# Performance work log

Hardware: AMD Instinct MI355X
Metric: run time of the kernel (lower is better)

## Reference

```python
import jax, jax.numpy as jnp
import numpy as np

B, S, C = 4, 2048, 1024
E, H = 1024, 16
D = E // H  # head_dim = 64


def setup_inputs() -> dict:
    key = jax.random.key(0)
    k1, k2, k3, k4, k5 = jax.random.split(key, 5)
    s = 1.0 / np.sqrt(C)
    return {
        "x": jax.random.normal(k1, (B, S, C), dtype=jnp.float32),
        "w_qkv": jax.random.uniform(k2, (C, 3 * E), minval=-s, maxval=s, dtype=jnp.float32),
        "b_qkv": jax.random.uniform(k3, (3 * E,), minval=-s, maxval=s, dtype=jnp.float32),
        "w_out": jax.random.uniform(k4, (E, E), minval=-1.0 / np.sqrt(E), maxval=1.0 / np.sqrt(E), dtype=jnp.float32),
        "b_out": jax.random.uniform(k5, (E,), minval=-1.0 / np.sqrt(E), maxval=1.0 / np.sqrt(E), dtype=jnp.float32),
    }


def reference(x, w_qkv, b_qkv, w_out, b_out):
    b, s, _ = x.shape
    qkv = x @ w_qkv + b_qkv                      # [B,S,3E]
    qkv = qkv.reshape(b, s, 3, H, D)
    q = qkv[:, :, 0].transpose(0, 2, 1, 3)       # [B,H,S,D]
    k = qkv[:, :, 1].transpose(0, 2, 1, 3)
    v = qkv[:, :, 2].transpose(0, 2, 1, 3)
    scale = jnp.asarray(D, x.dtype) ** 0.5
    scores = jnp.einsum("bhqd,bhkd->bhqk", q, k) / scale
    attn = jax.nn.softmax(scores, axis=-1)       # dropout is identity in eval mode
    out = jnp.einsum("bhqk,bhkd->bhqd", attn, v)
    out = out.transpose(0, 2, 1, 3).reshape(b, s, E)
    return out @ w_out + b_out
```

## Files before the change

### kernel.cpp

```cpp
#include <hip/hip_runtime.h>


typedef _Float16 f16;
typedef f16 f16x2 __attribute__((ext_vector_type(2)));
typedef f16 f16x4 __attribute__((ext_vector_type(4)));
typedef f16 f16x8 __attribute__((ext_vector_type(8)));
typedef float f32x4 __attribute__((ext_vector_type(4)));

typedef const __attribute__((address_space(1))) void* gas_ptr;
typedef __attribute__((address_space(3))) void* lds_ptr;

__device__ __forceinline__ void load_lds16(const void* g, void* s) {
  __builtin_amdgcn_global_load_lds((gas_ptr)g, (lds_ptr)s, 16, 0, 0);
}

__device__ __forceinline__ f32x4 mfma16(f16x8 a, f16x8 b, f32x4 c) {
  return __builtin_amdgcn_mfma_f32_16x16x32_f16(a, b, c, 0, 0, 0);
}

__device__ __forceinline__ f16x2 pk2(float a, float b) {
  return __builtin_bit_cast(f16x2, __builtin_amdgcn_cvt_pkrtz(a, b));
}

__global__ __launch_bounds__(256) void prep(const float* __restrict__ x, f16* __restrict__ xh,
                                            const float* __restrict__ w_qkv, f16* __restrict__ wqkvT,
                                            const float* __restrict__ w_out, f16* __restrict__ woutT) {
  __shared__ float t[32][33];
  int bid = blockIdx.x, tid = threadIdx.x;
  if (bid < 4096) {
    long i = (long)bid * 256 + tid;
    const float4* p = (const float4*)x;
    float4 a = p[2 * i], b = p[2 * i + 1];
    f16x8 o;
    o[0] = (f16)a.x; o[1] = (f16)a.y; o[2] = (f16)a.z; o[3] = (f16)a.w;
    o[4] = (f16)b.x; o[5] = (f16)b.y; o[6] = (f16)b.z; o[7] = (f16)b.w;
    *(f16x8*)(xh + 8 * i) = o;
    return;
  }
  const float* in;
  f16* out;
  int R, C, c0, r0;
  if (bid < 7168) {
    int r = bid - 4096;
    in = w_qkv; out = wqkvT; R = 1024; C = 3072;
    c0 = (r % 96) * 32; r0 = (r / 96) * 32;
  } else {
    int r = bid - 7168;
    in = w_out; out = woutT; R = 1024; C = 1024;
    c0 = (r & 31) * 32; r0 = (r >> 5) * 32;
  }
  int tx = tid & 31, ty = tid >> 5;
#pragma unroll
  for (int j = 0; j < 4; ++j)
    t[ty + 8 * j][tx] = in[(long)(r0 + ty + 8 * j) * C + c0 + tx];
  __syncthreads();
#pragma unroll
  for (int j = 0; j < 4; ++j)
    out[(long)(c0 + ty + 8 * j) * R + r0 + tx] = (f16)t[tx][ty + 8 * j];
}

__global__ __launch_bounds__(256) void qkv_gemm(const f16* __restrict__ A, const f16* __restrict__ BT,
                                                const float* __restrict__ bias,
                                                f16* __restrict__ Qs, f16* __restrict__ Kk,
                                                f16* __restrict__ Vt) {
  __shared__ __align__(16) f16 lA[2][128 * 64];
  __shared__ __align__(16) f16 lB[2][128 * 64];
  const int K = 1024;
  int tid = threadIdx.x, w = tid >> 6, lane = tid & 63, l16 = lane & 15, quad = lane >> 4;
  int wm = (w >> 1) * 64, wn = (w & 1) * 64;
  int id = blockIdx.y * gridDim.x + blockIdx.x;
  int xcd = id & 7, cch = id >> 3;
  int bx = xcd * 8 + (cch & 7), by = cch >> 3;
  int blockM = bx * 128, blockN = by * 128;
  int sw = l16 & 7;
  f32x4 acc[4][4] = {};

  auto stage = [&](int kt) {
    int k0 = kt * 64;
    f16* dA = lA[kt & 1];
    f16* dB = lB[kt & 1];
#pragma unroll
    for (int i = 0; i < 4; ++i) {
      int c = i * 256 + tid;
      int row = c >> 3;
      int sc = (c & 7) ^ (row & 7);
      load_lds16(A + (long)(blockM + row) * K + k0 + sc * 8, dA + c * 8);
      load_lds16(BT + (long)(blockN + row) * K + k0 + sc * 8, dB + c * 8);
    }
  };

  stage(0);
  asm volatile("s_waitcnt vmcnt(0)" ::: "memory");
  __builtin_amdgcn_s_barrier();

  for (int t = 0; t < 16; ++t) {
    if (t < 15) stage(t + 1);
    const f16* cA = lA[t & 1];
    const f16* cB = lB[t & 1];
#pragma unroll
    for (int ks = 0; ks < 2; ++ks) {
      f16x8 af[4], bf[4];
#pragma unroll
      for (int mb = 0; mb < 4; ++mb)
        af[mb] = *(const f16x8*)&cA[(wm + mb * 16 + l16) * 64 + ((ks * 4 + quad) ^ sw) * 8];
#pragma unroll
      for (int nb = 0; nb < 4; ++nb)
        bf[nb] = *(const f16x8*)&cB[(wn + nb * 16 + l16) * 64 + ((ks * 4 + quad) ^ sw) * 8];
      __builtin_amdgcn_s_setprio(1);
#pragma unroll
      for (int mb = 0; mb < 4; ++mb)
#pragma unroll
        for (int nb = 0; nb < 4; ++nb)
          acc[mb][nb] = mfma16(af[mb], bf[nb], acc[mb][nb]);
      __builtin_amdgcn_s_setprio(0);
    }
    asm volatile("s_waitcnt vmcnt(0)" ::: "memory");
    __builtin_amdgcn_s_barrier();
  }

  int which = by >> 3;
  const float SCALE = 0.18033688011112042f;
#pragma unroll
  for (int nb = 0; nb < 4; ++nb) {
    int col = blockN + wn + nb * 16 + l16;
    int hd = col & 1023, h = hd >> 6, d = hd & 63;
    float bv = bias[col];
#pragma unroll
    for (int mb = 0; mb < 4; ++mb) {
      int row0 = blockM + wm + mb * 16 + quad * 4;
      int b = row0 >> 11, s0 = row0 & 2047;
      if (which == 2) {
        f16x2 a = pk2(acc[mb][nb][0] + bv, acc[mb][nb][1] + bv);
        f16x2 c = pk2(acc[mb][nb][2] + bv, acc[mb][nb][3] + bv);
        *(f16x4*)&Vt[((b * 16 + h) * 64 + d) * 2048 + s0] =
            __builtin_shufflevector(a, c, 0, 1, 2, 3);
      } else if (which == 0) {
#pragma unroll
        for (int r = 0; r < 4; ++r)
          Qs[((b * 16 + h) * 2048 + s0 + r) * 64 + d] = (f16)((acc[mb][nb][r] + bv) * SCALE);
      } else {
#pragma unroll
        for (int r = 0; r < 4; ++r)
          Kk[((b * 16 + h) * 2048 + s0 + r) * 64 + d] = (f16)(acc[mb][nb][r] + bv);
      }
    }
  }
}

__global__ __launch_bounds__(512, 4) void attn(const f16* __restrict__ Qs, const f16* __restrict__ Kk,
                                               const f16* __restrict__ Vt, f16* __restrict__ ctx) {
  __shared__ __align__(16) f16 lK[2][64 * 64];
  __shared__ __align__(16) f16 lV[2][64 * 64];
  int id = blockIdx.y * gridDim.x + blockIdx.x;
  int swz = (id & 7) * 64 + (id >> 3);
  int qt = swz & 7, bh = swz >> 3;
  int tid = threadIdx.x, lane = tid & 63, l16 = lane & 15, quad = lane >> 4;
  int w = tid >> 6;
  int swr = l16 & 7;
  const f16* Qbase = Qs + ((long)bh * 2048 + qt * 256 + w * 32) * 64;
  const f16* Kbh = Kk + (long)bh * 2048 * 64;
  const f16* Vbh = Vt + (long)bh * 64 * 2048;

  f16x8 qf[2][2];
#pragma unroll
  for (int rb = 0; rb < 2; ++rb)
#pragma unroll
    for (int ks = 0; ks < 2; ++ks)
      qf[rb][ks] = *(const f16x8*)(Qbase + (rb * 16 + l16) * 64 + ks * 32 + quad * 8);

  f32x4 of[2][4] = {};
  f32x4 osum[2] = {};
  const f16 one = (f16)1.f;
  const f16x8 vone8 = {one, one, one, one, one, one, one, one};

  int rs = tid >> 3, o = (tid & 7) * 8, c1 = tid & 7;
  int jj = rs & 7;
  int koff = o & 31;
  int Lp = (o & 32) + ((koff & 12) << 1) + ((koff >> 4) << 2);
  int pv0b = (((Lp >> 3) ^ jj) << 4) + ((Lp & 4) << 1);
  int pv1b = ((((Lp >> 3) + 1) ^ jj) << 4) + ((Lp & 4) << 1);

  auto stageK = [&](int kt) {
    int kb0 = kt * 64;
    f16* dst = lK[kt & 1];
    load_lds16(Kbh + (kb0 + rs) * 64 + (c1 ^ jj) * 8, dst + tid * 8);
  };
  auto writeV = [&](int buf, float4 va) {
    f16* d0 = lV[buf] + rs * 64;
    f16x8 a8 = __builtin_bit_cast(f16x8, va);
    *(f16x4*)((char*)d0 + pv0b) = __builtin_shufflevector(a8, a8, 0, 1, 2, 3);
    *(f16x4*)((char*)d0 + pv1b) = __builtin_shufflevector(a8, a8, 4, 5, 6, 7);
  };

  {
    stageK(0);
    float4 va = *(const float4*)(Vbh + (long)rs * 2048 + o);
    writeV(0, va);
    asm volatile("s_waitcnt vmcnt(0)" ::: "memory");
    __builtin_amdgcn_s_barrier();
  }

  for (int kt = 0; kt < 32; ++kt) {
    int cur = kt & 1, nxt = cur ^ 1;

    float4 va;
    if (kt < 31) {
      int kb0 = (kt + 1) * 64;
      stageK(kt + 1);
      va = *(const float4*)(Vbh + (long)rs * 2048 + kb0 + o);
    }

    __builtin_amdgcn_s_setprio(1);
#pragma unroll
    for (int kp = 0; kp < 2; ++kp) {
      f16x4 pah[2][2];
#pragma unroll
      for (int kbh = 0; kbh < 2; ++kbh) {
        int kb = kp * 2 + kbh;
        f16x8 kf0 = *(const f16x8*)&lK[cur][(kb * 16 + l16) * 64 + ((quad ^ swr) << 3)];
        f16x8 kf1 = *(const f16x8*)&lK[cur][(kb * 16 + l16) * 64 + (((4 + quad) ^ swr) << 3)];
#pragma unroll
        for (int rb = 0; rb < 2; ++rb) {
          f32x4 z = {};
          z = mfma16(kf0, qf[rb][0], z);
          z = mfma16(kf1, qf[rb][1], z);
          float p0 = __builtin_amdgcn_exp2f(z[0]);
          float p1 = __builtin_amdgcn_exp2f(z[1]);
          float p2 = __builtin_amdgcn_exp2f(z[2]);
          float p3 = __builtin_amdgcn_exp2f(z[3]);
          pah[rb][kbh] = __builtin_shufflevector(pk2(p0, p1), pk2(p2, p3), 0, 1, 2, 3);
        }
      }
      f16x8 pa[2];
      pa[0] = __builtin_shufflevector(pah[0][0], pah[0][1], 0, 1, 2, 3, 4, 5, 6, 7);
      pa[1] = __builtin_shufflevector(pah[1][0], pah[1][1], 0, 1, 2, 3, 4, 5, 6, 7);

#pragma unroll
      for (int db = 0; db < 4; ++db) {
        f16x8 vf = *(const f16x8*)&lV[cur][(db * 16 + l16) * 64 + (((kp * 4 + quad) ^ swr) << 3)];
#pragma unroll
        for (int rb = 0; rb < 2; ++rb)
          of[rb][db] = mfma16(pa[rb], vf, of[rb][db]);
      }
#pragma unroll
      for (int rb = 0; rb < 2; ++rb)
        osum[rb] = mfma16(pa[rb], vone8, osum[rb]);
    }
    __builtin_amdgcn_s_setprio(0);

    if (kt < 31) {
      writeV(nxt, va);
      asm volatile("s_waitcnt vmcnt(0)" ::: "memory");
      __builtin_amdgcn_s_barrier();
    }
  }

  int b = bh >> 4, h = bh & 15;
  long token0 = (long)b * 2048 + qt * 256 + w * 32;
#pragma unroll
  for (int rb = 0; rb < 2; ++rb) {
    float inv[4];
#pragma unroll
    for (int r = 0; r < 4; ++r) inv[r] = 1.0f / osum[rb][r];
#pragma unroll
    for (int db = 0; db < 4; ++db)
#pragma unroll
      for (int r = 0; r < 4; ++r)
        ctx[(token0 + rb * 16 + quad * 4 + r) * 1024 + h * 64 + db * 16 + l16] =
            (f16)(of[rb][db][r] * inv[r]);
  }
}

__global__ __launch_bounds__(256) void proj_gemm(const f16* __restrict__ A, const f16* __restrict__ BT,
                                                 const float* __restrict__ bias,
                                                 float* __restrict__ out) {
  __shared__ __align__(16) f16 lA[2][128 * 64];
  __shared__ __align__(16) f16 lB[2][128 * 64];
  const int K = 1024;
  int tid = threadIdx.x, w = tid >> 6, lane = tid & 63, l16 = lane & 15, quad = lane >> 4;
  int wm = (w >> 1) * 64, wn = (w & 1) * 64;
  int id = blockIdx.y * gridDim.x + blockIdx.x;
  int xcd = id & 7, cch = id >> 3;
  int bx = xcd * 8 + (cch & 7), by = cch >> 3;
  int blockM = bx * 128, blockN = by * 128;
  int sw = l16 & 7;
  f32x4 acc[4][4] = {};

  auto stage = [&](int kt) {
    int k0 = kt * 64;
    f16* dA = lA[kt & 1];
    f16* dB = lB[kt & 1];
#pragma unroll
    for (int i = 0; i < 4; ++i) {
      int c = i * 256 + tid;
      int row = c >> 3;
      int sc = (c & 7) ^ (row & 7);
      load_lds16(A + (long)(blockM + row) * K + k0 + sc * 8, dA + c * 8);
      load_lds16(BT + (long)(blockN + row) * K + k0 + sc * 8, dB + c * 8);
    }
  };

  stage(0);
  asm volatile("s_waitcnt vmcnt(0)" ::: "memory");
  __builtin_amdgcn_s_barrier();

  for (int t = 0; t < 16; ++t) {
    if (t < 15) stage(t + 1);
    const f16* cA = lA[t & 1];
    const f16* cB = lB[t & 1];
#pragma unroll
    for (int ks = 0; ks < 2; ++ks) {
      f16x8 af[4], bf[4];
#pragma unroll
      for (int mb = 0; mb < 4; ++mb)
        af[mb] = *(const f16x8*)&cA[(wm + mb * 16 + l16) * 64 + ((ks * 4 + quad) ^ sw) * 8];
#pragma unroll
      for (int nb = 0; nb < 4; ++nb)
        bf[nb] = *(const f16x8*)&cB[(wn + nb * 16 + l16) * 64 + ((ks * 4 + quad) ^ sw) * 8];
      __builtin_amdgcn_s_setprio(1);
#pragma unroll
      for (int mb = 0; mb < 4; ++mb)
#pragma unroll
        for (int nb = 0; nb < 4; ++nb)
          acc[mb][nb] = mfma16(af[mb], bf[nb], acc[mb][nb]);
      __builtin_amdgcn_s_setprio(0);
    }
    asm volatile("s_waitcnt vmcnt(0)" ::: "memory");
    __builtin_amdgcn_s_barrier();
  }

#pragma unroll
  for (int nb = 0; nb < 4; ++nb) {
    int col = blockN + wn + nb * 16 + l16;
    float bv = bias[col];
#pragma unroll
    for (int mb = 0; mb < 4; ++mb) {
#pragma unroll
      for (int r = 0; r < 4; ++r) {
        int row = blockM + wm + mb * 16 + quad * 4 + r;
        out[(long)row * 1024 + col] = acc[mb][nb][r] + bv;
      }
    }
  }
}

extern "C" void kernel_launch(void* const* d_in, const int* in_sizes, int n_in,
                              void* d_out, int out_size, void* d_ws, size_t ws_size,
                              hipStream_t stream) {
  const float* x     = (const float*)d_in[0];
  const float* w_qkv = (const float*)d_in[1];
  const float* b_qkv = (const float*)d_in[2];
  const float* w_out = (const float*)d_in[3];
  const float* b_out = (const float*)d_in[4];
  float* out = (float*)d_out;

  char* ws = (char*)d_ws;
  f16* xh    = (f16*)(ws);
  f16* ctx   = (f16*)(ws);
  f16* wqkvT = (f16*)(ws + 16777216);
  f16* woutT = (f16*)(ws + 23068672);
  f16* Qs    = (f16*)(ws + 25165824);
  f16* Kk    = (f16*)(ws + 41943040);
  f16* Vt    = (f16*)(ws + 58720256);

  prep<<<8192, 256, 0, stream>>>(x, xh, w_qkv, wqkvT, w_out, woutT);
  qkv_gemm<<<dim3(64, 24), 256, 0, stream>>>(xh, wqkvT, b_qkv, Qs, Kk, Vt);
  attn<<<dim3(8, 64), 512, 0, stream>>>(Qs, Kk, Vt, ctx);
  proj_gemm<<<dim3(64, 8), 256, 0, stream>>>(ctx, woutT, b_out, out);
}
```

Measured before the change: 254.0 us.

## Use 8-wave blocks for GEMMs and 128-key tiles with register-staged K in attention

Both GEMM kernels now launch 512 threads per 128x128 tile, each wave computing a 32x64 sub-tile, to raise wave count and latency hiding. The attention kernel doubles its K/V tile to 128 keys, halving the number of loop iterations and barriers. It also replaces the direct global-to-LDS K load with register loads followed by LDS writes. The cost is more LDS per block, which may limit occupancy, and a longer register-held prefetch of four float4 values per thread.

```diff
diff --git a/kernel.cpp b/kernel.cpp
--- a/kernel.cpp
+++ b/kernel.cpp
@@ -59,29 +59,29 @@
     out[(long)(c0 + ty + 8 * j) * R + r0 + tx] = (f16)t[tx][ty + 8 * j];
 }
 
-__global__ __launch_bounds__(256) void qkv_gemm(const f16* __restrict__ A, const f16* __restrict__ BT,
-                                                const float* __restrict__ bias,
-                                                f16* __restrict__ Qs, f16* __restrict__ Kk,
-                                                f16* __restrict__ Vt) {
+__global__ __launch_bounds__(512, 4) void qkv_gemm(const f16* __restrict__ A, const f16* __restrict__ BT,
+                                                   const float* __restrict__ bias,
+                                                   f16* __restrict__ Qs, f16* __restrict__ Kk,
+                                                   f16* __restrict__ Vt) {
   __shared__ __align__(16) f16 lA[2][128 * 64];
   __shared__ __align__(16) f16 lB[2][128 * 64];
   const int K = 1024;
   int tid = threadIdx.x, w = tid >> 6, lane = tid & 63, l16 = lane & 15, quad = lane >> 4;
-  int wm = (w >> 1) * 64, wn = (w & 1) * 64;
+  int wm = (w >> 1) * 32, wn = (w & 1) * 64;
   int id = blockIdx.y * gridDim.x + blockIdx.x;
   int xcd = id & 7, cch = id >> 3;
   int bx = xcd * 8 + (cch & 7), by = cch >> 3;
   int blockM = bx * 128, blockN = by * 128;
   int sw = l16 & 7;
-  f32x4 acc[4][4] = {};
+  f32x4 acc[2][4] = {};
 
   auto stage = [&](int kt) {
     int k0 = kt * 64;
     f16* dA = lA[kt & 1];
     f16* dB = lB[kt & 1];
 #pragma unroll
-    for (int i = 0; i < 4; ++i) {
-      int c = i * 256 + tid;
+    for (int i = 0; i < 2; ++i) {
+      int c = i * 512 + tid;
       int row = c >> 3;
       int sc = (c & 7) ^ (row & 7);
       load_lds16(A + (long)(blockM + row) * K + k0 + sc * 8, dA + c * 8);
@@ -99,16 +99,16 @@
     const f16* cB = lB[t & 1];
 #pragma unroll
     for (int ks = 0; ks < 2; ++ks) {
-      f16x8 af[4], bf[4];
-#pragma unroll
-      for (int mb = 0; mb < 4; ++mb)
+      f16x8 af[2], bf[4];
+#pragma unroll
+      for (int mb = 0; mb < 2; ++mb)
         af[mb] = *(const f16x8*)&cA[(wm + mb * 16 + l16) * 64 + ((ks * 4 + quad) ^ sw) * 8];
 #pragma unroll
       for (int nb = 0; nb < 4; ++nb)
         bf[nb] = *(const f16x8*)&cB[(wn + nb * 16 + l16) * 64 + ((ks * 4 + quad) ^ sw) * 8];
       __builtin_amdgcn_s_setprio(1);
 #pragma unroll
-      for (int mb = 0; mb < 4; ++mb)
+      for (int mb = 0; mb < 2; ++mb)
 #pragma unroll
         for (int nb = 0; nb < 4; ++nb)
           acc[mb][nb] = mfma16(af[mb], bf[nb], acc[mb][nb]);
@@ -126,7 +126,7 @@
     int hd = col & 1023, h = hd >> 6, d = hd & 63;
     float bv = bias[col];
 #pragma unroll
-    for (int mb = 0; mb < 4; ++mb) {
+    for (int mb = 0; mb < 2; ++mb) {
       int row0 = blockM + wm + mb * 16 + quad * 4;
       int b = row0 >> 11, s0 = row0 & 2047;
       if (which == 2) {
@@ -149,8 +149,8 @@
 
 __global__ __launch_bounds__(512, 4) void attn(const f16* __restrict__ Qs, const f16* __restrict__ Kk,
                                                const f16* __restrict__ Vt, f16* __restrict__ ctx) {
-  __shared__ __align__(16) f16 lK[2][64 * 64];
-  __shared__ __align__(16) f16 lV[2][64 * 64];
+  __shared__ __align__(16) f16 lK[2][128 * 64];
+  __shared__ __align__(16) f16 lV[2][64 * 128];
   int id = blockIdx.y * gridDim.x + blockIdx.x;
   int swz = (id & 7) * 64 + (id >> 3);
   int qt = swz & 7, bh = swz >> 3;
@@ -173,46 +173,52 @@
   const f16 one = (f16)1.f;
   const f16x8 vone8 = {one, one, one, one, one, one, one, one};
 
-  int rs = tid >> 3, o = (tid & 7) * 8, c1 = tid & 7;
-  int jj = rs & 7;
+  int rk0 = tid >> 3, cl = tid & 7;
+  int jjk = rk0 & 7;
+  int kCl = (cl ^ jjk) * 8;
+  int dv0 = tid >> 4, ck = tid & 15, o = ck * 8;
+  int jjv = dv0 & 7;
   int koff = o & 31;
-  int Lp = (o & 32) + ((koff & 12) << 1) + ((koff >> 4) << 2);
-  int pv0b = (((Lp >> 3) ^ jj) << 4) + ((Lp & 4) << 1);
-  int pv1b = ((((Lp >> 3) + 1) ^ jj) << 4) + ((Lp & 4) << 1);
-
-  auto stageK = [&](int kt) {
-    int kb0 = kt * 64;
-    f16* dst = lK[kt & 1];
-    load_lds16(Kbh + (kb0 + rs) * 64 + (c1 ^ jj) * 8, dst + tid * 8);
+  int Lp = (o & 96) + ((koff & 12) << 1) + ((koff >> 4) << 2);
+  int pv0b = (((Lp >> 3) ^ jjv) << 4) + ((Lp & 4) << 1);
+  int pv1b = ((((Lp >> 3) + 1) ^ jjv) << 4) + ((Lp & 4) << 1);
+
+  auto loadKV = [&](int kt, float4& ka, float4& kb_, float4& va, float4& vb) {
+    int kb0 = kt * 128;
+    ka  = *(const float4*)(Kbh + (kb0 + rk0) * 64 + cl * 8);
+    kb_ = *(const float4*)(Kbh + (kb0 + rk0 + 64) * 64 + cl * 8);
+    va  = *(const float4*)(Vbh + (long)dv0 * 2048 + kb0 + o);
+    vb  = *(const float4*)(Vbh + (long)(dv0 + 32) * 2048 + kb0 + o);
   };
-  auto writeV = [&](int buf, float4 va) {
-    f16* d0 = lV[buf] + rs * 64;
+  auto writeKV = [&](int buf, float4 ka, float4 kb_, float4 va, float4 vb) {
+    *(f16x8*)&lK[buf][rk0 * 64 + kCl] = __builtin_bit_cast(f16x8, ka);
+    *(f16x8*)&lK[buf][(rk0 + 64) * 64 + kCl] = __builtin_bit_cast(f16x8, kb_);
+    char* d0 = (char*)(lV[buf] + dv0 * 128);
+    char* d1 = (char*)(lV[buf] + (dv0 + 32) * 128);
     f16x8 a8 = __builtin_bit_cast(f16x8, va);
-    *(f16x4*)((char*)d0 + pv0b) = __builtin_shufflevector(a8, a8, 0, 1, 2, 3);
-    *(f16x4*)((char*)d0 + pv1b) = __builtin_shufflevector(a8, a8, 4, 5, 6, 7);
+    f16x8 b8 = __builtin_bit_cast(f16x8, vb);
+    *(f16x4*)(d0 + pv0b) = __builtin_shufflevector(a8, a8, 0, 1, 2, 3);
+    *(f16x4*)(d0 + pv1b) = __builtin_shufflevector(a8, a8, 4, 5, 6, 7);
+    *(f16x4*)(d1 + pv0b) = __builtin_shufflevector(b8, b8, 0, 1, 2, 3);
+    *(f16x4*)(d1 + pv1b) = __builtin_shufflevector(b8, b8, 4, 5, 6, 7);
   };
 
   {
-    stageK(0);
-    float4 va = *(const float4*)(Vbh + (long)rs * 2048 + o);
-    writeV(0, va);
-    asm volatile("s_waitcnt vmcnt(0)" ::: "memory");
-    __builtin_amdgcn_s_barrier();
-  }
-
-  for (int kt = 0; kt < 32; ++kt) {
+    float4 ka, kb_, va, vb;
+    loadKV(0, ka, kb_, va, vb);
+    writeKV(0, ka, kb_, va, vb);
+  }
+  __syncthreads();
+
+  for (int kt = 0; kt < 16; ++kt) {
     int cur = kt & 1, nxt = cur ^ 1;
 
-    float4 va;
-    if (kt < 31) {
-      int kb0 = (kt + 1) * 64;
-      stageK(kt + 1);
-      va = *(const float4*)(Vbh + (long)rs * 2048 + kb0 + o);
-    }
+    float4 ka, kb_, va, vb;
+    if (kt < 15) loadKV(kt + 1, ka, kb_, va, vb);
 
     __builtin_amdgcn_s_setprio(1);
 #pragma unroll
-    for (int kp = 0; kp < 2; ++kp) {
+    for (int kp = 0; kp < 4; ++kp) {
       f16x4 pah[2][2];
 #pragma unroll
       for (int kbh = 0; kbh < 2; ++kbh) {
@@ -237,7 +243,7 @@
 
 #pragma unroll
       for (int db = 0; db < 4; ++db) {
-        f16x8 vf = *(const f16x8*)&lV[cur][(db * 16 + l16) * 64 + (((kp * 4 + quad) ^ swr) << 3)];
+        f16x8 vf = *(const f16x8*)&lV[cur][(db * 16 + l16) * 128 + (((kp * 4 + quad) ^ swr) << 3)];
 #pragma unroll
         for (int rb = 0; rb < 2; ++rb)
           of[rb][db] = mfma16(pa[rb], vf, of[rb][db]);
@@ -248,10 +254,9 @@
     }
     __builtin_amdgcn_s_setprio(0);
 
-    if (kt < 31) {
-      writeV(nxt, va);
-      asm volatile("s_waitcnt vmcnt(0)" ::: "memory");
-      __builtin_amdgcn_s_barrier();
+    if (kt < 15) {
+      writeKV(nxt, ka, kb_, va, vb);
+      __syncthreads();
     }
   }
 
@@ -271,28 +276,28 @@
   }
 }
 
-__global__ __launch_bounds__(256) void proj_gemm(const f16* __restrict__ A, const f16* __restrict__ BT,
-                                                 const float* __restrict__ bias,
-                                                 float* __restrict__ out) {
+__global__ __launch_bounds__(512, 4) void proj_gemm(const f16* __restrict__ A, const f16* __restrict__ BT,
+                                                    const float* __restrict__ bias,
+                                                    float* __restrict__ out) {
   __shared__ __align__(16) f16 lA[2][128 * 64];
   __shared__ __align__(16) f16 lB[2][128 * 64];
   const int K = 1024;
   int tid = threadIdx.x, w = tid >> 6, lane = tid & 63, l16 = lane & 15, quad = lane >> 4;
-  int wm = (w >> 1) * 64, wn = (w & 1) * 64;
+  int wm = (w >> 1) * 32, wn = (w & 1) * 64;
   int id = blockIdx.y * gridDim.x + blockIdx.x;
   int xcd = id & 7, cch = id >> 3;
   int bx = xcd * 8 + (cch & 7), by = cch >> 3;
   int blockM = bx * 128, blockN = by * 128;
   int sw = l16 & 7;
-  f32x4 acc[4][4] = {};
+  f32x4 acc[2][4] = {};
 
   auto stage = [&](int kt) {
     int k0 = kt * 64;
     f16* dA = lA[kt & 1];
     f16* dB = lB[kt & 1];
 #pragma unroll
-    for (int i = 0; i < 4; ++i) {
-      int c = i * 256 + tid;
+    for (int i = 0; i < 2; ++i) {
+      int c = i * 512 + tid;
       int row = c >> 3;
       int sc = (c & 7) ^ (row & 7);
       load_lds16(A + (long)(blockM + row) * K + k0 + sc * 8, dA + c * 8);
@@ -310,16 +315,16 @@
     const f16* cB = lB[t & 1];
 #pragma unroll
     for (int ks = 0; ks < 2; ++ks) {
-      f16x8 af[4], bf[4];
-#pragma unroll
-      for (int mb = 0; mb < 4; ++mb)
+      f16x8 af[2], bf[4];
+#pragma unroll
+      for (int mb = 0; mb < 2; ++mb)
         af[mb] = *(const f16x8*)&cA[(wm + mb * 16 + l16) * 64 + ((ks * 4 + quad) ^ sw) * 8];
 #pragma unroll
       for (int nb = 0; nb < 4; ++nb)
         bf[nb] = *(const f16x8*)&cB[(wn + nb * 16 + l16) * 64 + ((ks * 4 + quad) ^ sw) * 8];
       __builtin_amdgcn_s_setprio(1);
 #pragma unroll
-      for (int mb = 0; mb < 4; ++mb)
+      for (int mb = 0; mb < 2; ++mb)
 #pragma unroll
         for (int nb = 0; nb < 4; ++nb)
           acc[mb][nb] = mfma16(af[mb], bf[nb], acc[mb][nb]);
@@ -334,7 +339,7 @@
     int col = blockN + wn + nb * 16 + l16;
     float bv = bias[col];
 #pragma unroll
-    for (int mb = 0; mb < 4; ++mb) {
+    for (int mb = 0; mb < 2; ++mb) {
 #pragma unroll
       for (int r = 0; r < 4; ++r) {
         int row = blockM + wm + mb * 16 + quad * 4 + r;
@@ -364,7 +369,7 @@
   f16* Vt    = (f16*)(ws + 58720256);
 
   prep<<<8192, 256, 0, stream>>>(x, xh, w_qkv, wqkvT, w_out, woutT);
-  qkv_gemm<<<dim3(64, 24), 256, 0, stream>>>(xh, wqkvT, b_qkv, Qs, Kk, Vt);
+  qkv_gemm<<<dim3(64, 24), 512, 0, stream>>>(xh, wqkvT, b_qkv, Qs, Kk, Vt);
   attn<<<dim3(8, 64), 512, 0, stream>>>(Qs, Kk, Vt, ctx);
-  proj_gemm<<<dim3(64, 8), 256, 0, stream>>>(ctx, woutT, b_out, out);
-}
+  proj_gemm<<<dim3(64, 8), 512, 0, stream>>>(ctx, woutT, b_out, out);
+}
```

Measured after the change: 244.0 us. 3.9% less time.
